# Kernel optimization log

Hardware: AMD Instinct MI355X
Metric: run time of the kernel (lower is better)

Reference implementation:

```python
import jax, jax.numpy as jnp
import numpy as np

EPS = 1e-15        # norm / denominator clamp (matches geoopt min_norm)
BALL_EPS = 1e-5    # projection margin: max radius = (1-BALL_EPS)/sqrt(c)
TANH_ARG_MAX = 15.0  # pre-expmap tangent clip so tanh arg stays finite
ATANH_MAX = 1.0 - 1e-7

def _norm(x):
    return jnp.maximum(jnp.linalg.norm(x, axis=-1, keepdims=True), EPS)

def pre_clip(x, c):
    # clip tangent norm so sqrt(c)*||x|| <= TANH_ARG_MAX before expmap0
    maxn = TANH_ARG_MAX / jnp.sqrt(c)
    n = _norm(x)
    return x * jnp.minimum(1.0, maxn / n)

def post_clip(x, c):
    # project onto the open Poincare ball of curvature c
    maxn = (1.0 - BALL_EPS) / jnp.sqrt(c)
    n = _norm(x)
    return x * jnp.minimum(1.0, maxn / n)

def expmap0(u, c):
    sc = jnp.sqrt(c)
    n = _norm(u)
    return jnp.tanh(sc * n) * u / (sc * n)

def logmap0(y, c):
    sc = jnp.sqrt(c)
    n = _norm(y)
    return jnp.arctanh(jnp.minimum(sc * n, ATANH_MAX)) * y / (sc * n)

def mobius_add(x, y, c):
    x2 = jnp.sum(x * x, axis=-1, keepdims=True)
    y2 = jnp.sum(y * y, axis=-1, keepdims=True)
    xy = jnp.sum(x * y, axis=-1, keepdims=True)
    num = (1.0 + 2.0 * c * xy + c * y2) * x + (1.0 - c * x2) * y
    den = 1.0 + 2.0 * c * xy + (c * c) * x2 * y2
    return num / jnp.maximum(den, EPS)

def mobius_scalar_mul(r, x, c):
    sc = jnp.sqrt(c)
    n = _norm(x)
    return jnp.tanh(r * jnp.arctanh(jnp.minimum(sc * n, ATANH_MAX))) * x / (sc * n)


def setup_inputs() -> dict:
    key = jax.random.key(0)
    kx, ky = jax.random.split(key)
    B, N, D = 64, 577, 768
    # scale so points land well inside the ball after expmap0
    x = jax.random.normal(kx, (B, N, D), dtype=jnp.float32) * 0.05
    y = jax.random.normal(ky, (B, N, D), dtype=jnp.float32) * 0.05
    return {
        "x": x,
        "y": y,
        "curv_hra": jnp.asarray(np.log(np.e - 1.0), dtype=jnp.float32),  # inv_softplus(1.0)
        "gamma_raw": jnp.asarray(0.5, dtype=jnp.float32),
        "gamma_scale": jnp.asarray(0.0, dtype=jnp.float32),
        "scale_center": jnp.asarray(0.0, dtype=jnp.float32),
    }


def reference(x, y, curv_hra, gamma_raw, gamma_scale, scale_center):
    c = jax.nn.softplus(curv_hra)  # ball curvature from raw param
    hr_x = post_clip(expmap0(pre_clip(x, c), c), c)
    hr_y = post_clip(expmap0(pre_clip(y, c), c), c)
    s = jax.nn.sigmoid(scale_center)
    g_max = 1.0 + jax.nn.softplus(gamma_scale)
    gamma = g_max * jnp.tanh(gamma_raw)
    # learned Mobius midpoint p between hr_x and hr_y
    sx = post_clip(mobius_scalar_mul(s, hr_x, c), c)
    sy = post_clip(mobius_scalar_mul(1.0 - s, hr_y, c), c)
    p = post_clip(mobius_add(sx, sy, c), c)
    # recenter at p, scale residual branch, add, move back, log to tangent
    x_p = post_clip(mobius_add(-p, hr_x, c), c)
    y_p = post_clip(mobius_add(-p, hr_y, c), c)
    y_s = post_clip(mobius_scalar_mul(gamma, y_p, c), c)
    hres_p = post_clip(mobius_add(x_p, y_s, c), c)
    hres = mobius_add(p, hres_p, c)
    r = post_clip(hres, c)
    return logmap0(r, c)
```

## Files before the change

kernel.cpp:

```cpp
#include <hip/hip_runtime.h>
#include <math.h>

#define F_EPS 1e-15f
#define F_BALL_EPS 1e-5f
#define F_TANH_ARG_MAX 15.0f
#define F_ATANH_MAX (1.0f - 1e-7f)
#define F_LOG2E 1.4426950408889634f
#define F_LN2   0.6931471805599453f

__device__ __forceinline__ float rcp_fast(float x) {
    float r = __builtin_amdgcn_rcpf(x);
    return r * (2.0f - x * r);
}
__device__ __forceinline__ float div_fast(float a, float b) { return a * rcp_fast(b); }
__device__ __forceinline__ float sqrt_fast(float x) { return __builtin_amdgcn_sqrtf(x); }
__device__ __forceinline__ float exp2_fast(float x) { return __builtin_amdgcn_exp2f(x); }
__device__ __forceinline__ float log2_fast(float x) { return __builtin_amdgcn_logf(x); }
__device__ __forceinline__ float exp_fast(float x)  { return exp2_fast(x * F_LOG2E); }

__device__ __forceinline__ float tanh_fast(float x) {
    float ax = fabsf(x);
    float t  = exp2_fast(ax * (-2.0f * F_LOG2E));
    float r  = (1.0f - t) * rcp_fast(1.0f + t);
    return copysignf(r, x);
}
__device__ __forceinline__ float atanh_fast(float z) {
    return (0.5f * F_LN2) * log2_fast((1.0f + z) * rcp_fast(1.0f - z));
}
__device__ __forceinline__ float softplus_fast(float x) {
    return F_LN2 * log2_fast(1.0f + exp2_fast(x * F_LOG2E));
}

struct Gram { float X2, Y2, XY; };

__device__ __forceinline__ float wave_sum(float v) {
#pragma unroll
    for (int o = 32; o > 0; o >>= 1) v += __shfl_xor(v, o, 64);
    return v;
}

__device__ __forceinline__ float g_norm2(const Gram& g, float a, float b) {
    return fmaxf(a * a * g.X2 + 2.0f * a * b * g.XY + b * b * g.Y2, 0.0f);
}
__device__ __forceinline__ float g_norm(const Gram& g, float a, float b) {
    return fmaxf(sqrt_fast(g_norm2(g, a, b)), F_EPS);
}
__device__ __forceinline__ float g_dot(const Gram& g, float au, float bu, float av, float bv) {
    return au * av * g.X2 + (au * bv + bu * av) * g.XY + bu * bv * g.Y2;
}

__device__ __forceinline__ void g_postclip(const Gram& g, float maxn, float& a, float& b) {
    float n = g_norm(g, a, b);
    float s = fminf(1.0f, div_fast(maxn, n));
    a *= s; b *= s;
}

__device__ __forceinline__ void g_msm(const Gram& g, float sc, float r, float& a, float& b) {
    float n = g_norm(g, a, b);
    float z = fminf(sc * n, F_ATANH_MAX);
    float f = tanh_fast(r * atanh_fast(z)) * rcp_fast(sc * n);
    a *= f; b *= f;
}

__device__ __forceinline__ void g_madd(const Gram& g, float c,
                                       float au, float bu, float av, float bv,
                                       float& ao, float& bo) {
    float u2 = g_norm2(g, au, bu);
    float v2 = g_norm2(g, av, bv);
    float uv = g_dot(g, au, bu, av, bv);
    float A = 1.0f + 2.0f * c * uv + c * v2;
    float B = 1.0f - c * u2;
    float rden = rcp_fast(fmaxf(1.0f + 2.0f * c * uv + c * c * u2 * v2, F_EPS));
    ao = (A * au + B * av) * rden;
    bo = (A * bu + B * bv) * rden;
}

__device__ __forceinline__ float hr_coeff(float n, float sc, float maxn_pre, float maxn_post) {
    float s1 = fminf(1.0f, div_fast(maxn_pre, n));
    float n1 = fmaxf(s1 * n, F_EPS);
    float f1 = tanh_fast(sc * n1) * rcp_fast(sc * n1);
    float a  = s1 * f1;
    float n2 = fmaxf(fabsf(a) * n, F_EPS);
    float s2 = fminf(1.0f, div_fast(maxn_post, n2));
    return a * s2;
}

__global__ __launch_bounds__(256) void hra_kernel(
    const float* __restrict__ x, const float* __restrict__ y,
    const float* __restrict__ p_curv, const float* __restrict__ p_graw,
    const float* __restrict__ p_gscale, const float* __restrict__ p_scent,
    float* __restrict__ out, int rows)
{
    const int wave = (blockIdx.x << 2) | (threadIdx.x >> 6);
    const int lane = threadIdx.x & 63;
    if (wave >= rows) return;

    const float4* xr = (const float4*)(x + (size_t)wave * 768);
    const float4* yr = (const float4*)(y + (size_t)wave * 768);
    float4* outr = (float4*)(out + (size_t)wave * 768);

    float4 xv[3], yv[3];
#pragma unroll
    for (int j = 0; j < 3; j++) {
        xv[j] = xr[lane + 64 * j];
        yv[j] = yr[lane + 64 * j];
    }

    float sxx = 0.0f, syy = 0.0f, sxy = 0.0f;
#pragma unroll
    for (int j = 0; j < 3; j++) {
        sxx += xv[j].x * xv[j].x + xv[j].y * xv[j].y + xv[j].z * xv[j].z + xv[j].w * xv[j].w;
        syy += yv[j].x * yv[j].x + yv[j].y * yv[j].y + yv[j].z * yv[j].z + yv[j].w * yv[j].w;
        sxy += xv[j].x * yv[j].x + xv[j].y * yv[j].y + xv[j].z * yv[j].z + xv[j].w * yv[j].w;
    }
    Gram g;
    g.X2 = wave_sum(sxx);
    g.Y2 = wave_sum(syy);
    g.XY = wave_sum(sxy);

    const float curv   = p_curv[0];
    const float graw   = p_graw[0];
    const float gscale = p_gscale[0];
    const float scent  = p_scent[0];

    const float c  = softplus_fast(curv);
    const float sc = sqrt_fast(c);
    const float maxn_pre  = div_fast(F_TANH_ARG_MAX, sc);
    const float maxn_post = div_fast(1.0f - F_BALL_EPS, sc);

    const float s     = rcp_fast(1.0f + exp_fast(-scent));
    const float g_max = 1.0f + softplus_fast(gscale);
    const float gamma = g_max * tanh_fast(graw);

    const float nx = fmaxf(sqrt_fast(g.X2), F_EPS);
    const float ny = fmaxf(sqrt_fast(g.Y2), F_EPS);

    const float hx = hr_coeff(nx, sc, maxn_pre, maxn_post);
    const float hy = hr_coeff(ny, sc, maxn_pre, maxn_post);

    float sxa = hx, sxb = 0.0f;
    g_msm(g, sc, s, sxa, sxb);
    g_postclip(g, maxn_post, sxa, sxb);

    float sya = 0.0f, syb = hy;
    g_msm(g, sc, 1.0f - s, sya, syb);
    g_postclip(g, maxn_post, sya, syb);

    float pa, pb;
    g_madd(g, c, sxa, sxb, sya, syb, pa, pb);
    g_postclip(g, maxn_post, pa, pb);

    float xpa, xpb;
    g_madd(g, c, -pa, -pb, hx, 0.0f, xpa, xpb);
    g_postclip(g, maxn_post, xpa, xpb);

    float ypa, ypb;
    g_madd(g, c, -pa, -pb, 0.0f, hy, ypa, ypb);
    g_postclip(g, maxn_post, ypa, ypb);

    g_msm(g, sc, gamma, ypa, ypb);
    g_postclip(g, maxn_post, ypa, ypb);

    float ha, hb;
    g_madd(g, c, xpa, xpb, ypa, ypb, ha, hb);
    g_postclip(g, maxn_post, ha, hb);

    float ra, rb;
    g_madd(g, c, pa, pb, ha, hb, ra, rb);
    g_postclip(g, maxn_post, ra, rb);

    float nr = g_norm(g, ra, rb);
    float z  = fminf(sc * nr, F_ATANH_MAX);
    float f  = atanh_fast(z) * rcp_fast(sc * nr);

    const float fa = f * ra;
    const float fb = f * rb;

#pragma unroll
    for (int j = 0; j < 3; j++) {
        float4 o;
        o.x = fa * xv[j].x + fb * yv[j].x;
        o.y = fa * xv[j].y + fb * yv[j].y;
        o.z = fa * xv[j].z + fb * yv[j].z;
        o.w = fa * xv[j].w + fb * yv[j].w;
        outr[lane + 64 * j] = o;
    }
}

extern "C" void kernel_launch(void* const* d_in, const int* in_sizes, int n_in,
                              void* d_out, int out_size, void* d_ws, size_t ws_size,
                              hipStream_t stream) {
    const float* x = (const float*)d_in[0];
    const float* y = (const float*)d_in[1];
    const float* curv = (const float*)d_in[2];
    const float* graw = (const float*)d_in[3];
    const float* gscale = (const float*)d_in[4];
    const float* scent = (const float*)d_in[5];
    float* out = (float*)d_out;

    const int rows = in_sizes[0] / 768;
    const int blocks = (rows + 3) / 4;

    hipLaunchKernelGGL(hra_kernel, dim3(blocks), dim3(256), 0, stream,
                       x, y, curv, graw, gscale, scent, out, rows);
}
```

Baseline: 277.8 us.

## Process four rows per wave and compute each row's scalar chain on separate lanes

```diff
diff --git a/kernel.cpp b/kernel.cpp
--- a/kernel.cpp
+++ b/kernel.cpp
@@ -32,12 +32,6 @@
 }
 
 struct Gram { float X2, Y2, XY; };
-
-__device__ __forceinline__ float wave_sum(float v) {
-#pragma unroll
-    for (int o = 32; o > 0; o >>= 1) v += __shfl_xor(v, o, 64);
-    return v;
-}
 
 __device__ __forceinline__ float g_norm2(const Gram& g, float a, float b) {
     return fmaxf(a * a * g.X2 + 2.0f * a * b * g.XY + b * b * g.Y2, 0.0f);
@@ -85,7 +79,56 @@
     return a * s2;
 }
 
-__global__ __launch_bounds__(256) void hra_kernel(
+__device__ __forceinline__ void row_chain(const Gram& g,
+                                          float c, float sc, float maxn_pre, float maxn_post,
+                                          float s, float gamma,
+                                          float& fa, float& fb) {
+    const float nx = fmaxf(sqrt_fast(g.X2), F_EPS);
+    const float ny = fmaxf(sqrt_fast(g.Y2), F_EPS);
+
+    const float hx = hr_coeff(nx, sc, maxn_pre, maxn_post);
+    const float hy = hr_coeff(ny, sc, maxn_pre, maxn_post);
+
+    float sxa = hx, sxb = 0.0f;
+    g_msm(g, sc, s, sxa, sxb);
+    g_postclip(g, maxn_post, sxa, sxb);
+
+    float sya = 0.0f, syb = hy;
+    g_msm(g, sc, 1.0f - s, sya, syb);
+    g_postclip(g, maxn_post, sya, syb);
+
+    float pa, pb;
+    g_madd(g, c, sxa, sxb, sya, syb, pa, pb);
+    g_postclip(g, maxn_post, pa, pb);
+
+    float xpa, xpb;
+    g_madd(g, c, -pa, -pb, hx, 0.0f, xpa, xpb);
+    g_postclip(g, maxn_post, xpa, xpb);
+
+    float ypa, ypb;
+    g_madd(g, c, -pa, -pb, 0.0f, hy, ypa, ypb);
+    g_postclip(g, maxn_post, ypa, ypb);
+
+    g_msm(g, sc, gamma, ypa, ypb);
+    g_postclip(g, maxn_post, ypa, ypb);
+
+    float ha, hb;
+    g_madd(g, c, xpa, xpb, ypa, ypb, ha, hb);
+    g_postclip(g, maxn_post, ha, hb);
+
+    float ra, rb;
+    g_madd(g, c, pa, pb, ha, hb, ra, rb);
+    g_postclip(g, maxn_post, ra, rb);
+
+    float nr = g_norm(g, ra, rb);
+    float z  = fminf(sc * nr, F_ATANH_MAX);
+    float f  = atanh_fast(z) * rcp_fast(sc * nr);
+
+    fa = f * ra;
+    fb = f * rb;
+}
+
+__global__ __launch_bounds__(256, 3) void hra_kernel(
     const float* __restrict__ x, const float* __restrict__ y,
     const float* __restrict__ p_curv, const float* __restrict__ p_graw,
     const float* __restrict__ p_gscale, const float* __restrict__ p_scent,
@@ -93,97 +136,80 @@
 {
     const int wave = (blockIdx.x << 2) | (threadIdx.x >> 6);
     const int lane = threadIdx.x & 63;
-    if (wave >= rows) return;
-
-    const float4* xr = (const float4*)(x + (size_t)wave * 768);
-    const float4* yr = (const float4*)(y + (size_t)wave * 768);
-    float4* outr = (float4*)(out + (size_t)wave * 768);
-
-    float4 xv[3], yv[3];
-#pragma unroll
-    for (int j = 0; j < 3; j++) {
-        xv[j] = xr[lane + 64 * j];
-        yv[j] = yr[lane + 64 * j];
-    }
-
-    float sxx = 0.0f, syy = 0.0f, sxy = 0.0f;
-#pragma unroll
-    for (int j = 0; j < 3; j++) {
-        sxx += xv[j].x * xv[j].x + xv[j].y * xv[j].y + xv[j].z * xv[j].z + xv[j].w * xv[j].w;
-        syy += yv[j].x * yv[j].x + yv[j].y * yv[j].y + yv[j].z * yv[j].z + yv[j].w * yv[j].w;
-        sxy += xv[j].x * yv[j].x + xv[j].y * yv[j].y + xv[j].z * yv[j].z + xv[j].w * yv[j].w;
-    }
+    const int base = wave << 2;
+    if (base >= rows) return;
+
+    float4 xv[4][3], yv[4][3];
+#pragma unroll
+    for (int r = 0; r < 4; r++) {
+        const float4* xr = (const float4*)(x) + (size_t)(base + r) * 192;
+        const float4* yr = (const float4*)(y) + (size_t)(base + r) * 192;
+#pragma unroll
+        for (int j = 0; j < 3; j++) {
+            xv[r][j] = xr[lane + 64 * j];
+            yv[r][j] = yr[lane + 64 * j];
+        }
+    }
+
+    float sxx[4], syy[4], sxy[4];
+#pragma unroll
+    for (int r = 0; r < 4; r++) {
+        float a = 0.0f, b = 0.0f, d = 0.0f;
+#pragma unroll
+        for (int j = 0; j < 3; j++) {
+            a += xv[r][j].x * xv[r][j].x + xv[r][j].y * xv[r][j].y + xv[r][j].z * xv[r][j].z + xv[r][j].w * xv[r][j].w;
+            b += yv[r][j].x * yv[r][j].x + yv[r][j].y * yv[r][j].y + yv[r][j].z * yv[r][j].z + yv[r][j].w * yv[r][j].w;
+            d += xv[r][j].x * yv[r][j].x + xv[r][j].y * yv[r][j].y + xv[r][j].z * yv[r][j].z + xv[r][j].w * yv[r][j].w;
+        }
+        sxx[r] = a; syy[r] = b; sxy[r] = d;
+    }
+
+#pragma unroll
+    for (int o = 32; o > 0; o >>= 1) {
+#pragma unroll
+        for (int r = 0; r < 4; r++) {
+            sxx[r] += __shfl_xor(sxx[r], o, 64);
+            syy[r] += __shfl_xor(syy[r], o, 64);
+            sxy[r] += __shfl_xor(sxy[r], o, 64);
+        }
+    }
+
+    const int rsel = lane & 3;
     Gram g;
-    g.X2 = wave_sum(sxx);
-    g.Y2 = wave_sum(syy);
-    g.XY = wave_sum(sxy);
-
-    const float curv   = p_curv[0];
-    const float graw   = p_graw[0];
-    const float gscale = p_gscale[0];
-    const float scent  = p_scent[0];
-
-    const float c  = softplus_fast(curv);
+    g.X2 = (rsel < 2) ? (rsel == 0 ? sxx[0] : sxx[1]) : (rsel == 2 ? sxx[2] : sxx[3]);
+    g.Y2 = (rsel < 2) ? (rsel == 0 ? syy[0] : syy[1]) : (rsel == 2 ? syy[2] : syy[3]);
+    g.XY = (rsel < 2) ? (rsel == 0 ? sxy[0] : sxy[1]) : (rsel == 2 ? sxy[2] : sxy[3]);
+
+    const float c  = softplus_fast(p_curv[0]);
     const float sc = sqrt_fast(c);
     const float maxn_pre  = div_fast(F_TANH_ARG_MAX, sc);
     const float maxn_post = div_fast(1.0f - F_BALL_EPS, sc);
-
-    const float s     = rcp_fast(1.0f + exp_fast(-scent));
-    const float g_max = 1.0f + softplus_fast(gscale);
-    const float gamma = g_max * tanh_fast(graw);
-
-    const float nx = fmaxf(sqrt_fast(g.X2), F_EPS);
-    const float ny = fmaxf(sqrt_fast(g.Y2), F_EPS);
-
-    const float hx = hr_coeff(nx, sc, maxn_pre, maxn_post);
-    const float hy = hr_coeff(ny, sc, maxn_pre, maxn_post);
-
-    float sxa = hx, sxb = 0.0f;
-    g_msm(g, sc, s, sxa, sxb);
-    g_postclip(g, maxn_post, sxa, sxb);
-
-    float sya = 0.0f, syb = hy;
-    g_msm(g, sc, 1.0f - s, sya, syb);
-    g_postclip(g, maxn_post, sya, syb);
-
-    float pa, pb;
-    g_madd(g, c, sxa, sxb, sya, syb, pa, pb);
-    g_postclip(g, maxn_post, pa, pb);
-
-    float xpa, xpb;
-    g_madd(g, c, -pa, -pb, hx, 0.0f, xpa, xpb);
-    g_postclip(g, maxn_post, xpa, xpb);
-
-    float ypa, ypb;
-    g_madd(g, c, -pa, -pb, 0.0f, hy, ypa, ypb);
-    g_postclip(g, maxn_post, ypa, ypb);
-
-    g_msm(g, sc, gamma, ypa, ypb);
-    g_postclip(g, maxn_post, ypa, ypb);
-
-    float ha, hb;
-    g_madd(g, c, xpa, xpb, ypa, ypb, ha, hb);
-    g_postclip(g, maxn_post, ha, hb);
-
-    float ra, rb;
-    g_madd(g, c, pa, pb, ha, hb, ra, rb);
-    g_postclip(g, maxn_post, ra, rb);
-
-    float nr = g_norm(g, ra, rb);
-    float z  = fminf(sc * nr, F_ATANH_MAX);
-    float f  = atanh_fast(z) * rcp_fast(sc * nr);
-
-    const float fa = f * ra;
-    const float fb = f * rb;
-
-#pragma unroll
-    for (int j = 0; j < 3; j++) {
-        float4 o;
-        o.x = fa * xv[j].x + fb * yv[j].x;
-        o.y = fa * xv[j].y + fb * yv[j].y;
-        o.z = fa * xv[j].z + fb * yv[j].z;
-        o.w = fa * xv[j].w + fb * yv[j].w;
-        outr[lane + 64 * j] = o;
+    const float s     = rcp_fast(1.0f + exp_fast(-p_scent[0]));
+    const float g_max = 1.0f + softplus_fast(p_gscale[0]);
+    const float gamma = g_max * tanh_fast(p_graw[0]);
+
+    float fa, fb;
+    row_chain(g, c, sc, maxn_pre, maxn_post, s, gamma, fa, fb);
+
+    float far[4], fbr[4];
+#pragma unroll
+    for (int r = 0; r < 4; r++) {
+        far[r] = __shfl(fa, r, 64);
+        fbr[r] = __shfl(fb, r, 64);
+    }
+
+#pragma unroll
+    for (int r = 0; r < 4; r++) {
+        float4* outr = (float4*)(out) + (size_t)(base + r) * 192;
+#pragma unroll
+        for (int j = 0; j < 3; j++) {
+            float4 o;
+            o.x = far[r] * xv[r][j].x + fbr[r] * yv[r][j].x;
+            o.y = far[r] * xv[r][j].y + fbr[r] * yv[r][j].y;
+            o.z = far[r] * xv[r][j].z + fbr[r] * yv[r][j].z;
+            o.w = far[r] * xv[r][j].w + fbr[r] * yv[r][j].w;
+            outr[lane + 64 * j] = o;
+        }
     }
 }
 
@@ -199,7 +225,8 @@
     float* out = (float*)d_out;
 
     const int rows = in_sizes[0] / 768;
-    const int blocks = (rows + 3) / 4;
+    const int waves = (rows + 3) / 4;
+    const int blocks = (waves + 3) / 4;
 
     hipLaunchKernelGGL(hra_kernel, dim3(blocks), dim3(256), 0, stream,
                        x, y, curv, graw, gscale, scent, out, rows);
```

New measurement: 282.1 us. No clear change (+1.6%).
